# Performance work log

Measured on AMD Instinct MI355X. Metric: run time of the kernel, lower is better.

The kernel has to match this reference:

```python
import jax, jax.numpy as jnp
import numpy as np

B = 8192
N_INPUTS = 16 * 12 * 64  # 12288, FEATURE_FACTORIZE=False
H0, H1, H2 = 256, 32, 32
OUTPUT_SCALE = 300.0
WDL_SCALE = 200.0
AVG_ACTIVE = 30.0  # ~30 active features per position (NNUE sparsity)


def setup_inputs() -> dict:
    key = jax.random.key(0)
    ks = jax.random.split(key, 11)
    p = AVG_ACTIVE / N_INPUTS
    # near-one-hot sparse binary feature vectors, as produced by get_features()
    wf = (jax.random.uniform(ks[0], (B, N_INPUTS)) < p).astype(jnp.float32)
    bf = (jax.random.uniform(ks[1], (B, N_INPUTS)) < p).astype(jnp.float32)
    side = jax.random.randint(ks[2], (B,), 0, 2).astype(jnp.bool_)
    qs1, qs2, qs3 = float(1 << 6), float(1 << 6), float(1 << 5)
    ft_w = jax.random.normal(ks[3], (H0, N_INPUTS), jnp.float32) * jnp.sqrt(2.0 / N_INPUTS)
    ft_b = jax.random.normal(ks[4], (H0,), jnp.float32) * 0.5
    l1_w = jax.random.normal(ks[5], (H1, 2 * H0), jnp.float32) * (32.0 / qs1)
    l1_b = jax.random.normal(ks[6], (H1,), jnp.float32) * 0.5
    l2_w = jax.random.normal(ks[7], (H2, H1), jnp.float32) * (32.0 / qs2)
    l2_b = jax.random.normal(ks[8], (H2,), jnp.float32) * 0.5
    l3_w = jax.random.normal(ks[9], (1, H2), jnp.float32) * (2048.0 / (OUTPUT_SCALE * qs3))
    l3_b = jax.random.normal(ks[10], (1,), jnp.float32) * 0.5
    return {"white_features": wf, "black_features": bf, "side": side,
            "ft_w": ft_w, "ft_b": ft_b, "l1_w": l1_w, "l1_b": l1_b,
            "l2_w": l2_w, "l2_b": l2_b, "l3_w": l3_w, "l3_b": l3_b}


def reference(white_features, black_features, side, ft_w, ft_b,
              l1_w, l1_b, l2_w, l2_b, l3_w, l3_b):
    # feature transformer on each perspective: [B, H0]
    w = white_features @ ft_w.T + ft_b
    b = black_features @ ft_w.T + ft_b
    s = side[:, None]
    # side-to-move perspective first: [B, 2*H0]
    acc = jnp.where(s, jnp.concatenate([w, b], axis=1),
                    jnp.concatenate([b, w], axis=1))
    o0 = jnp.clip(acc, 0.0, 1.0)
    o1 = jnp.clip(o0 @ l1_w.T + l1_b, 0.0, 1.0)
    o2 = jnp.clip(o1 @ l2_w.T + l2_b, 0.0, 1.0)
    o3 = (o2 @ l3_w.T + l3_b) * OUTPUT_SCALE  # [B, 1]
    return jax.nn.sigmoid(o3 / WDL_SCALE)
```

## Files before the change

kernel.cpp:

```cpp
#include <hip/hip_runtime.h>
#include <math.h>

#define NB 8192
#define NI 12288
#define H0 256
#define H1 32
#define H2 32
#define SEGCAP 96
#define OUT_SCALE 300.0f
#define WDL_SCALE 200.0f

typedef float          f32x4 __attribute__((ext_vector_type(4)));
typedef unsigned short u16x4 __attribute__((ext_vector_type(4)));

#define FTT_B  ((size_t)NI * H0 * 2)
#define WS_NEED FTT_B

__device__ __forceinline__ unsigned short f2bf(float f) {
    unsigned u = __float_as_uint(f);
    u += 0x7FFFu + ((u >> 16) & 1u);
    return (unsigned short)(u >> 16);
}
__device__ __forceinline__ f32x4 bf4_to_f32(u16x4 h) {
    f32x4 r;
    r.x = __uint_as_float(((unsigned)h.x) << 16);
    r.y = __uint_as_float(((unsigned)h.y) << 16);
    r.z = __uint_as_float(((unsigned)h.z) << 16);
    r.w = __uint_as_float(((unsigned)h.w) << 16);
    return r;
}

__global__ __launch_bounds__(256) void nnue_ft_transpose_bf16(
    const float* __restrict__ src, unsigned short* __restrict__ dst)
{
    __shared__ float tile[64][65];
    const int bx = blockIdx.x, by = blockIdx.y;
    const int tx = threadIdx.x, ty = threadIdx.y;
    const int col = bx * 64 + tx;
    for (int j = ty; j < 64; j += 4)
        tile[j][tx] = src[(size_t)(by * 64 + j) * NI + col];
    __syncthreads();
    const int h = by * 64 + tx;
    for (int j = ty; j < 64; j += 4)
        dst[(size_t)(bx * 64 + j) * H0 + h] = f2bf(tile[tx][j]);
}

__global__ __launch_bounds__(256) void nnue_fwd(
    const float* __restrict__ wf, const float* __restrict__ bf,
    const int* __restrict__ side,
    const unsigned short* __restrict__ ftb16,
    const float* __restrict__ ft_b,
    const float* __restrict__ l1_w, const float* __restrict__ l1_b,
    const float* __restrict__ l2_w, const float* __restrict__ l2_b,
    const float* __restrict__ l3_w, const float* __restrict__ l3_b,
    float* __restrict__ out)
{
    __shared__ int   seg[4][2][SEGCAP];
    __shared__ float pacc[4][2][H0] __attribute__((aligned(16)));
    __shared__ float o0[2 * H0];
    __shared__ float o1[H1];

    const int row = blockIdx.x;
    const int t   = threadIdx.x;
    const int w   = t >> 6;
    const int l   = t & 63;
    const unsigned short* ftl = ftb16 + 4 * l;
    const unsigned long long ltmask = (1ull << l) - 1ull;

    const f32x4* wf4 = (const f32x4*)(wf + (size_t)row * NI);
    const f32x4* bf4 = (const f32x4*)(bf + (size_t)row * NI);

    #define BALLOT4(vec, kk, lst, n) { \
        const int ebase = (t + (kk) * 256) * 4; \
        { const bool nz = ((vec).x != 0.f); const unsigned long long mk = __ballot(nz); \
          if (mk) { const int pos = __popcll(mk & ltmask); \
                    if (nz && n + pos < SEGCAP) lst[n + pos] = ebase + 0; n += __popcll(mk); } } \
        { const bool nz = ((vec).y != 0.f); const unsigned long long mk = __ballot(nz); \
          if (mk) { const int pos = __popcll(mk & ltmask); \
                    if (nz && n + pos < SEGCAP) lst[n + pos] = ebase + 1; n += __popcll(mk); } } \
        { const bool nz = ((vec).z != 0.f); const unsigned long long mk = __ballot(nz); \
          if (mk) { const int pos = __popcll(mk & ltmask); \
                    if (nz && n + pos < SEGCAP) lst[n + pos] = ebase + 2; n += __popcll(mk); } } \
        { const bool nz = ((vec).w != 0.f); const unsigned long long mk = __ballot(nz); \
          if (mk) { const int pos = __popcll(mk & ltmask); \
                    if (nz && n + pos < SEGCAP) lst[n + pos] = ebase + 3; n += __popcll(mk); } } }

    int nW = 0;
    {
        int* lst = seg[w][0];
        f32x4 v[8];
        #pragma unroll
        for (int k = 0; k < 8; ++k)
            v[k] = __builtin_nontemporal_load(&wf4[t + k * 256]);
        #pragma unroll
        for (int k = 0; k < 4; ++k) BALLOT4(v[k], k, lst, nW)
        #pragma unroll
        for (int k = 0; k < 4; ++k)
            v[k] = __builtin_nontemporal_load(&wf4[t + (8 + k) * 256]);
        #pragma unroll
        for (int k = 4; k < 8; ++k) BALLOT4(v[k], k, lst, nW)
        #pragma unroll
        for (int k = 0; k < 4; ++k) BALLOT4(v[k], 8 + k, lst, nW)
        if (nW > SEGCAP) nW = SEGCAP;
    }

    f32x4 u[8];
    #pragma unroll
    for (int k = 0; k < 8; ++k)
        u[k] = __builtin_nontemporal_load(&bf4[t + k * 256]);

    {
        f32x4 a0 = {0.f,0.f,0.f,0.f}, a1 = a0, a2 = a0, a3 = a0;
        int i = 0;
        for (; i + 4 <= nW; i += 4) {
            const int i0 = __builtin_amdgcn_readfirstlane(seg[w][0][i]);
            const int i1 = __builtin_amdgcn_readfirstlane(seg[w][0][i + 1]);
            const int i2 = __builtin_amdgcn_readfirstlane(seg[w][0][i + 2]);
            const int i3 = __builtin_amdgcn_readfirstlane(seg[w][0][i + 3]);
            a0 += bf4_to_f32(*(const u16x4*)(ftl + (size_t)i0 * H0));
            a1 += bf4_to_f32(*(const u16x4*)(ftl + (size_t)i1 * H0));
            a2 += bf4_to_f32(*(const u16x4*)(ftl + (size_t)i2 * H0));
            a3 += bf4_to_f32(*(const u16x4*)(ftl + (size_t)i3 * H0));
        }
        for (; i < nW; ++i) {
            const int i0 = __builtin_amdgcn_readfirstlane(seg[w][0][i]);
            a0 += bf4_to_f32(*(const u16x4*)(ftl + (size_t)i0 * H0));
        }
        *(f32x4*)&pacc[w][0][4 * l] = (a0 + a1) + (a2 + a3);
    }

    int nB = 0;
    {
        int* lst = seg[w][1];
        #pragma unroll
        for (int k = 0; k < 4; ++k) BALLOT4(u[k], k, lst, nB)
        #pragma unroll
        for (int k = 0; k < 4; ++k)
            u[k] = __builtin_nontemporal_load(&bf4[t + (8 + k) * 256]);
        #pragma unroll
        for (int k = 4; k < 8; ++k) BALLOT4(u[k], k, lst, nB)
        #pragma unroll
        for (int k = 0; k < 4; ++k) BALLOT4(u[k], 8 + k, lst, nB)
        if (nB > SEGCAP) nB = SEGCAP;
    }
    #undef BALLOT4

    {
        f32x4 b0 = {0.f,0.f,0.f,0.f}, b1 = b0, b2 = b0, b3 = b0;
        int i = 0;
        for (; i + 4 <= nB; i += 4) {
            const int i0 = __builtin_amdgcn_readfirstlane(seg[w][1][i]);
            const int i1 = __builtin_amdgcn_readfirstlane(seg[w][1][i + 1]);
            const int i2 = __builtin_amdgcn_readfirstlane(seg[w][1][i + 2]);
            const int i3 = __builtin_amdgcn_readfirstlane(seg[w][1][i + 3]);
            b0 += bf4_to_f32(*(const u16x4*)(ftl + (size_t)i0 * H0));
            b1 += bf4_to_f32(*(const u16x4*)(ftl + (size_t)i1 * H0));
            b2 += bf4_to_f32(*(const u16x4*)(ftl + (size_t)i2 * H0));
            b3 += bf4_to_f32(*(const u16x4*)(ftl + (size_t)i3 * H0));
        }
        for (; i < nB; ++i) {
            const int i0 = __builtin_amdgcn_readfirstlane(seg[w][1][i]);
            b0 += bf4_to_f32(*(const u16x4*)(ftl + (size_t)i0 * H0));
        }
        *(f32x4*)&pacc[w][1][4 * l] = (b0 + b1) + (b2 + b3);
    }
    __syncthreads();

    {
        const float ftb  = ft_b[t];
        const float accW = ftb + ((pacc[0][0][t] + pacc[1][0][t]) + (pacc[2][0][t] + pacc[3][0][t]));
        const float accB = ftb + ((pacc[0][1][t] + pacc[1][1][t]) + (pacc[2][1][t] + pacc[3][1][t]));
        const bool s = side[row] != 0;
        const float wv = fminf(fmaxf(accW, 0.f), 1.f);
        const float bv = fminf(fmaxf(accB, 0.f), 1.f);
        o0[t]      = s ? wv : bv;
        o0[t + H0] = s ? bv : wv;
    }
    __syncthreads();

    {
        const int j = t >> 3, p = t & 7;
        const float* wrow = l1_w + j * (2 * H0);
        float sum = 0.f;
        #pragma unroll
        for (int m2 = 0; m2 < 64; ++m2) {
            const int k = p + 8 * m2;
            sum += wrow[k] * o0[k];
        }
        sum += __shfl_xor(sum, 1);
        sum += __shfl_xor(sum, 2);
        sum += __shfl_xor(sum, 4);
        if (p == 0) o1[j] = fminf(fmaxf(sum + l1_b[j], 0.f), 1.f);
    }
    __syncthreads();

    if (t < 32) {
        const float* wrow = l2_w + t * H1;
        float sum2 = 0.f;
        #pragma unroll
        for (int k = 0; k < H1; ++k) sum2 += wrow[k] * o1[k];
        const float o2v = fminf(fmaxf(sum2 + l2_b[t], 0.f), 1.f);
        float part = o2v * l3_w[t];
        part += __shfl_xor(part, 1);
        part += __shfl_xor(part, 2);
        part += __shfl_xor(part, 4);
        part += __shfl_xor(part, 8);
        part += __shfl_xor(part, 16);
        if (t == 0) {
            const float o3 = (part + l3_b[0]) * OUT_SCALE;
            out[row] = 1.f / (1.f + __expf(-o3 / WDL_SCALE));
        }
    }
}

__global__ __launch_bounds__(256) void nnue_fused_fallback(
    const float* __restrict__ wf, const float* __restrict__ bf,
    const int* __restrict__ side,
    const float* __restrict__ ft,
    const float* __restrict__ ft_b,
    const float* __restrict__ l1_w, const float* __restrict__ l1_b,
    const float* __restrict__ l2_w, const float* __restrict__ l2_b,
    const float* __restrict__ l3_w, const float* __restrict__ l3_b,
    float* __restrict__ out)
{
    __shared__ int   idxW[256], idxB[256];
    __shared__ int   cnts[2];
    __shared__ float o0[2 * H0];
    __shared__ float o1[H1];

    const int row = blockIdx.x;
    const int t   = threadIdx.x;
    if (t < 2) cnts[t] = 0;
    __syncthreads();

    const f32x4* wf4 = (const f32x4*)(wf + (size_t)row * NI);
    const f32x4* bf4 = (const f32x4*)(bf + (size_t)row * NI);
    const float ftb = ft_b[t];

    for (int half = 0; half < 2; ++half) {
        const f32x4* p4 = half ? bf4 : wf4;
        int* lst = half ? idxB : idxW;
        f32x4 v[12];
        #pragma unroll
        for (int k = 0; k < 12; ++k)
            v[k] = __builtin_nontemporal_load(&p4[t + k * 256]);
        #pragma unroll
        for (int k = 0; k < 12; ++k) {
            const int base = (t + k * 256) * 4;
            int m = (v[k].x != 0.f ? 1 : 0) | (v[k].y != 0.f ? 2 : 0)
                  | (v[k].z != 0.f ? 4 : 0) | (v[k].w != 0.f ? 8 : 0);
            while (m) {
                const int b = __ffs(m) - 1;
                m &= m - 1;
                lst[atomicAdd(&cnts[half], 1)] = base + b;
            }
        }
    }
    __syncthreads();

    const int nW = cnts[0], nB = cnts[1];
    float accW = ftb, accB = ftb;
    const float* ftr = ft + (size_t)t * NI;
    for (int j = 0; j < nW; ++j) accW += ftr[idxW[j]];
    for (int j = 0; j < nB; ++j) accB += ftr[idxB[j]];

    const bool s = side[row] != 0;
    const float wv = fminf(fmaxf(accW, 0.f), 1.f);
    const float bv = fminf(fmaxf(accB, 0.f), 1.f);
    o0[t]      = s ? wv : bv;
    o0[t + H0] = s ? bv : wv;
    __syncthreads();

    {
        const int j = t >> 3, p = t & 7;
        const float* wrow = l1_w + j * (2 * H0);
        float sum = 0.f;
        #pragma unroll
        for (int m = 0; m < 64; ++m) sum += wrow[p + 8 * m] * o0[p + 8 * m];
        sum += __shfl_xor(sum, 1);
        sum += __shfl_xor(sum, 2);
        sum += __shfl_xor(sum, 4);
        if (p == 0) o1[j] = fminf(fmaxf(sum + l1_b[j], 0.f), 1.f);
    }
    __syncthreads();

    if (t < 32) {
        const float* wrow = l2_w + t * H1;
        float sum2 = 0.f;
        #pragma unroll
        for (int k = 0; k < H1; ++k) sum2 += wrow[k] * o1[k];
        const float o2v = fminf(fmaxf(sum2 + l2_b[t], 0.f), 1.f);
        float part = o2v * l3_w[t];
        part += __shfl_xor(part, 1);
        part += __shfl_xor(part, 2);
        part += __shfl_xor(part, 4);
        part += __shfl_xor(part, 8);
        part += __shfl_xor(part, 16);
        if (t == 0) {
            const float o3 = (part + l3_b[0]) * OUT_SCALE;
            out[row] = 1.f / (1.f + __expf(-o3 / WDL_SCALE));
        }
    }
}

extern "C" void kernel_launch(void* const* d_in, const int* in_sizes, int n_in,
                              void* d_out, int out_size, void* d_ws, size_t ws_size,
                              hipStream_t stream) {
    const float* wf   = (const float*)d_in[0];
    const float* bf   = (const float*)d_in[1];
    const int*   side = (const int*)d_in[2];
    const float* ft_w = (const float*)d_in[3];
    const float* ft_b = (const float*)d_in[4];
    const float* l1_w = (const float*)d_in[5];
    const float* l1_b = (const float*)d_in[6];
    const float* l2_w = (const float*)d_in[7];
    const float* l2_b = (const float*)d_in[8];
    const float* l3_w = (const float*)d_in[9];
    const float* l3_b = (const float*)d_in[10];
    float*       out  = (float*)d_out;

    if (ws_size >= WS_NEED) {
        unsigned short* ftT = (unsigned short*)d_ws;
        nnue_ft_transpose_bf16<<<dim3(NI / 64, H0 / 64), dim3(64, 4), 0, stream>>>(ft_w, ftT);
        nnue_fwd<<<NB, 256, 0, stream>>>(wf, bf, side, ftT, ft_b,
                                         l1_w, l1_b, l2_w, l2_b, l3_w, l3_b, out);
    } else {
        nnue_fused_fallback<<<NB, 256, 0, stream>>>(wf, bf, side, ft_w, ft_b,
                                                    l1_w, l1_b, l2_w, l2_b,
                                                    l3_w, l3_b, out);
    }
}
```

Before: 163.1 us.

## Stream dense feature rows through LDS with double-buffered global_load_lds

Replaces the register-staged nontemporal loads of the dense white and black feature rows with direct global-to-LDS loads (global_load_lds, 16 bytes per lane) into a per-wave double buffer. Each step waits on vmcnt, reads one chunk from LDS, ballots the nonzero indices, then issues the load two chunks ahead. The intent is to cut VGPR pressure and keep loads in flight during the scan. The risk is that only two chunks are outstanding per wave instead of up to eight, which lowers memory-level parallelism on a bandwidth-bound streaming read, and the hand-written waitcnt asm adds an extra LDS round trip.

```diff
diff --git a/kernel.cpp b/kernel.cpp
--- a/kernel.cpp
+++ b/kernel.cpp
@@ -15,6 +15,9 @@
 
 #define FTT_B  ((size_t)NI * H0 * 2)
 #define WS_NEED FTT_B
+
+#define GAS __attribute__((address_space(1)))
+#define LAS __attribute__((address_space(3)))
 
 __device__ __forceinline__ unsigned short f2bf(float f) {
     unsigned u = __float_as_uint(f);
@@ -55,6 +58,7 @@
     const float* __restrict__ l3_w, const float* __restrict__ l3_b,
     float* __restrict__ out)
 {
+    __shared__ float sbuf[4][2][256] __attribute__((aligned(16)));
     __shared__ int   seg[4][2][SEGCAP];
     __shared__ float pacc[4][2][H0] __attribute__((aligned(16)));
     __shared__ float o0[2 * H0];
@@ -69,6 +73,11 @@
 
     const f32x4* wf4 = (const f32x4*)(wf + (size_t)row * NI);
     const f32x4* bf4 = (const f32x4*)(bf + (size_t)row * NI);
+
+    #define GLL(SRC4, c, buf) \
+        __builtin_amdgcn_global_load_lds( \
+            (const GAS void*)((SRC4) + (c) * 256 + t), \
+            (LAS void*)(&sbuf[w][buf][0]), 16, 0, 0);
 
     #define BALLOT4(vec, kk, lst, n) { \
         const int ebase = (t + (kk) * 256) * 4; \
@@ -85,29 +94,29 @@
           if (mk) { const int pos = __popcll(mk & ltmask); \
                     if (nz && n + pos < SEGCAP) lst[n + pos] = ebase + 3; n += __popcll(mk); } } }
 
+    #define STEP(SRC4, c, WL, lst, n) { \
+        asm volatile("s_waitcnt vmcnt(" WL ")" ::: "memory"); \
+        const f32x4 vv = *(const f32x4*)&sbuf[w][(c) & 1][l * 4]; \
+        asm volatile("s_waitcnt lgkmcnt(0)" ::: "memory"); \
+        BALLOT4(vv, c, lst, n) \
+        if ((c) + 2 < 12) { GLL(SRC4, (c) + 2, ((c) + 2) & 1) } }
+
     int nW = 0;
     {
         int* lst = seg[w][0];
-        f32x4 v[8];
-        #pragma unroll
-        for (int k = 0; k < 8; ++k)
-            v[k] = __builtin_nontemporal_load(&wf4[t + k * 256]);
-        #pragma unroll
-        for (int k = 0; k < 4; ++k) BALLOT4(v[k], k, lst, nW)
-        #pragma unroll
-        for (int k = 0; k < 4; ++k)
-            v[k] = __builtin_nontemporal_load(&wf4[t + (8 + k) * 256]);
-        #pragma unroll
-        for (int k = 4; k < 8; ++k) BALLOT4(v[k], k, lst, nW)
-        #pragma unroll
-        for (int k = 0; k < 4; ++k) BALLOT4(v[k], 8 + k, lst, nW)
+        GLL(wf4, 0, 0)
+        GLL(wf4, 1, 1)
+        STEP(wf4, 0,  "1", lst, nW) STEP(wf4, 1,  "1", lst, nW)
+        STEP(wf4, 2,  "1", lst, nW) STEP(wf4, 3,  "1", lst, nW)
+        STEP(wf4, 4,  "1", lst, nW) STEP(wf4, 5,  "1", lst, nW)
+        STEP(wf4, 6,  "1", lst, nW) STEP(wf4, 7,  "1", lst, nW)
+        STEP(wf4, 8,  "1", lst, nW) STEP(wf4, 9,  "1", lst, nW)
+        STEP(wf4, 10, "1", lst, nW) STEP(wf4, 11, "0", lst, nW)
         if (nW > SEGCAP) nW = SEGCAP;
     }
 
-    f32x4 u[8];
-    #pragma unroll
-    for (int k = 0; k < 8; ++k)
-        u[k] = __builtin_nontemporal_load(&bf4[t + k * 256]);
+    GLL(bf4, 0, 0)
+    GLL(bf4, 1, 1)
 
     {
         f32x4 a0 = {0.f,0.f,0.f,0.f}, a1 = a0, a2 = a0, a3 = a0;
@@ -132,18 +141,17 @@
     int nB = 0;
     {
         int* lst = seg[w][1];
-        #pragma unroll
-        for (int k = 0; k < 4; ++k) BALLOT4(u[k], k, lst, nB)
-        #pragma unroll
-        for (int k = 0; k < 4; ++k)
-            u[k] = __builtin_nontemporal_load(&bf4[t + (8 + k) * 256]);
-        #pragma unroll
-        for (int k = 4; k < 8; ++k) BALLOT4(u[k], k, lst, nB)
-        #pragma unroll
-        for (int k = 0; k < 4; ++k) BALLOT4(u[k], 8 + k, lst, nB)
+        STEP(bf4, 0,  "1", lst, nB) STEP(bf4, 1,  "1", lst, nB)
+        STEP(bf4, 2,  "1", lst, nB) STEP(bf4, 3,  "1", lst, nB)
+        STEP(bf4, 4,  "1", lst, nB) STEP(bf4, 5,  "1", lst, nB)
+        STEP(bf4, 6,  "1", lst, nB) STEP(bf4, 7,  "1", lst, nB)
+        STEP(bf4, 8,  "1", lst, nB) STEP(bf4, 9,  "1", lst, nB)
+        STEP(bf4, 10, "1", lst, nB) STEP(bf4, 11, "0", lst, nB)
         if (nB > SEGCAP) nB = SEGCAP;
     }
+    #undef STEP
     #undef BALLOT4
+    #undef GLL
 
     {
         f32x4 b0 = {0.f,0.f,0.f,0.f}, b1 = b0, b2 = b0, b3 = b0;
```

Result: slower. 185.3 us (+13.6%).
